# Kernel tuning notes

Measured on AMD Instinct MI355X. Metric: run time of the kernel, lower is better.

The kernel has to match this reference:

```python
import jax, jax.numpy as jnp
import numpy as np

N, E, D_IN, D_HID, D_OUT, R, B = 50000, 600000, 128, 128, 128, 8, 4


def setup_inputs() -> dict:
    key = jax.random.key(0)
    ks = jax.random.split(key, 12)
    s = 0.05
    return {
        "x": jax.random.normal(ks[0], (N, D_IN), jnp.float32),
        "edge_index": jax.random.randint(ks[1], (2, E), 0, N, jnp.int32),
        "edge_type": jax.random.randint(ks[2], (E,), 0, R, jnp.int32),
        "basis1": jax.random.normal(ks[3], (B, D_IN, D_HID), jnp.float32) * s,
        "comp1": jax.random.normal(ks[4], (R, B), jnp.float32) * s,
        "root1": jax.random.normal(ks[5], (D_IN, D_HID), jnp.float32) * s,
        "bias1": jnp.zeros((D_HID,), jnp.float32),
        "basis2": jax.random.normal(ks[6], (B, D_HID, D_OUT), jnp.float32) * s,
        "comp2": jax.random.normal(ks[7], (R, B), jnp.float32) * s,
        "root2": jax.random.normal(ks[8], (D_HID, D_OUT), jnp.float32) * s,
        "bias2": jnp.zeros((D_OUT,), jnp.float32),
    }


def _rgcn_conv(x, src, dst, etype, basis, comp, root, bias):
    # PyG RGCNConv (basis decomposition, aggr='mean' per relation):
    # out_i = x_i @ root + bias + sum_r mean_{e: type=r, dst=i} (x_src_e @ W_r)
    # W_r linear => aggregate raw features per (node, relation), then transform.
    n = x.shape[0]
    r = comp.shape[0]
    W = jnp.einsum('rb,bio->rio', comp, basis)          # [R, in, out]
    seg = dst * r + etype                               # [E] composite key
    agg = jax.ops.segment_sum(x[src], seg, num_segments=n * r)        # [N*R, in]
    cnt = jax.ops.segment_sum(jnp.ones_like(seg, x.dtype), seg, num_segments=n * r)
    mean = (agg / jnp.maximum(cnt, 1.0)[:, None]).reshape(n, r, -1)   # [N, R, in]
    return jnp.einsum('nri,rio->no', mean, W) + x @ root + bias


def reference(x, edge_index, edge_type, basis1, comp1, root1, bias1,
              basis2, comp2, root2, bias2):
    src, dst = edge_index[0], edge_index[1]
    h = _rgcn_conv(x, src, dst, edge_type, basis1, comp1, root1, bias1)
    h = jax.nn.relu(h)
    # dropout p=0.2 is identity in eval mode
    out = _rgcn_conv(h, src, dst, edge_type, basis2, comp2, root2, bias2)
    return out
```

## Files before the change

kernel.cpp:

```cpp
#include <hip/hip_runtime.h>

#define NN 50000
#define NE 600000
#define DD 128
#define RR 8
#define NBASIS 4
#define NR (NN * RR)
#define KTOT 640
#define MPAD 50048

typedef float f32x4 __attribute__((ext_vector_type(4)));
typedef short bf16x8 __attribute__((ext_vector_type(8)));

static __device__ __forceinline__ unsigned short f2b(float f) {
  union { float f; unsigned u; } c; c.f = f;
  unsigned u = c.u + 0x7fffu + ((c.u >> 16) & 1u);
  return (unsigned short)(u >> 16);
}
static __device__ __forceinline__ unsigned pack2(float lo, float hi) {
  return (unsigned)f2b(lo) | ((unsigned)f2b(hi) << 16);
}
static __device__ __forceinline__ float b2f_lo(unsigned v) {
  union { unsigned u; float f; } c; c.u = v << 16; return c.f;
}
static __device__ __forceinline__ float b2f_hi(unsigned v) {
  union { unsigned u; float f; } c; c.u = v & 0xffff0000u; return c.f;
}

__global__ __launch_bounds__(256) void count_kernel(
    const int* __restrict__ dst, const int* __restrict__ et,
    int* __restrict__ cnt) {
  int e = blockIdx.x * 256 + threadIdx.x;
  if (e < NE) atomicAdd(&cnt[dst[e] * RR + et[e]], 1);
}

__global__ __launch_bounds__(256) void scan1_kernel(
    const int* __restrict__ cnt, int* __restrict__ deg,
    int* __restrict__ offs, int* __restrict__ partials) {
  __shared__ int s[256];
  int t = threadIdx.x;
  int i = blockIdx.x * 256 + t;
  int v = 0;
  if (i < NN) {
    const int4* c4 = (const int4*)cnt;
    int4 a = c4[i * 2];
    int4 b = c4[i * 2 + 1];
    v = a.x + a.y + a.z + a.w + b.x + b.y + b.z + b.w;
    deg[i] = v;
  }
  s[t] = v;
  __syncthreads();
  for (int off = 1; off < 256; off <<= 1) {
    int add = (t >= off) ? s[t - off] : 0;
    __syncthreads();
    s[t] += add;
    __syncthreads();
  }
  if (i < NN) offs[i] = s[t] - v;
  if (t == 255) partials[blockIdx.x] = s[255];
}

__global__ __launch_bounds__(256) void scan2_kernel(
    int* __restrict__ partials, int nb) {
  __shared__ int s[256];
  int t = threadIdx.x;
  int v = (t < nb) ? partials[t] : 0;
  s[t] = v;
  __syncthreads();
  for (int off = 1; off < 256; off <<= 1) {
    int add = (t >= off) ? s[t - off] : 0;
    __syncthreads();
    s[t] += add;
    __syncthreads();
  }
  if (t < nb) partials[t] = s[t] - v;
}

__global__ __launch_bounds__(256) void scan3_kernel(
    int* __restrict__ offs, const int* __restrict__ partials,
    int* __restrict__ cursor) {
  int i = blockIdx.x * 256 + threadIdx.x;
  if (i < NN) {
    int o = offs[i] + partials[blockIdx.x];
    offs[i] = o;
    cursor[i] = o;
  }
}

__global__ __launch_bounds__(256) void sort_kernel(
    const int* __restrict__ src, const int* __restrict__ dst,
    const int* __restrict__ et, const int* __restrict__ cnt,
    int* __restrict__ cursor, int* __restrict__ skey,
    float* __restrict__ sinv) {
  int e = blockIdx.x * 256 + threadIdx.x;
  if (e >= NE) return;
  int d = dst[e];
  int t = et[e];
  int p = atomicAdd(&cursor[d], 1);
  skey[p] = src[e] | (t << 28);
  sinv[p] = 1.0f / (float)cnt[d * RR + t];
}

__global__ __launch_bounds__(256) void scv_kernel(
    const int* __restrict__ skey, const float* __restrict__ sinv,
    const float* __restrict__ comp1, const float* __restrict__ comp2,
    float4* __restrict__ scv1, float4* __restrict__ scv2) {
  int e = blockIdx.x * 256 + threadIdx.x;
  if (e >= NE) return;
  int t = ((unsigned)skey[e]) >> 28;
  float iv = sinv[e];
  scv1[e] = make_float4(iv * comp1[t * NBASIS + 0], iv * comp1[t * NBASIS + 1],
                        iv * comp1[t * NBASIS + 2], iv * comp1[t * NBASIS + 3]);
  scv2[e] = make_float4(iv * comp2[t * NBASIS + 0], iv * comp2[t * NBASIS + 1],
                        iv * comp2[t * NBASIS + 2], iv * comp2[t * NBASIS + 3]);
}

__global__ __launch_bounds__(256) void tobf16_kernel(
    const float* __restrict__ in, unsigned* __restrict__ outb, int npairs) {
  int i = blockIdx.x * 256 + threadIdx.x;
  if (i < npairs) {
    float2 v = ((const float2*)in)[i];
    outb[i] = pack2(v.x, v.y);
  }
}

__global__ __launch_bounds__(256) void btbuild_kernel(
    const float* __restrict__ basis, const float* __restrict__ root,
    unsigned short* __restrict__ BT) {
  int idx = blockIdx.x * 256 + threadIdx.x;
  if (idx >= DD * KTOT) return;
  int c = idx / KTOT;
  int k = idx - c * KTOT;
  float v = (k < 512) ? basis[(size_t)((k >> 7) * DD + (k & 127)) * DD + c]
                      : root[(size_t)(k - 512) * DD + c];
  BT[idx] = f2b(v);
}

__global__ __launch_bounds__(256) void agg_kernel(
    const uint4* __restrict__ featb4,
    const int* __restrict__ skey, const float4* __restrict__ scv,
    const int* __restrict__ offs, const int* __restrict__ deg,
    uint4* __restrict__ Ab4) {
  int node = blockIdx.x * 4 + (threadIdx.x >> 6);
  if (node >= NN) return;
  int lane = threadIdx.x & 63;
  int g = lane >> 4;
  int q = lane & 15;

  float a0[8] = {}, a1[8] = {}, a2[8] = {}, a3[8] = {};

  int beg = offs[node];
  int dg = deg[node];
  for (int i = g; i < dg; i += 4) {
    int key = skey[beg + i];
    int s = key & 0x0FFFFFFF;
    float4 c = scv[beg + i];
    uint4 v = featb4[(size_t)s * 16 + q];
    float e[8];
    e[0] = b2f_lo(v.x); e[1] = b2f_hi(v.x);
    e[2] = b2f_lo(v.y); e[3] = b2f_hi(v.y);
    e[4] = b2f_lo(v.z); e[5] = b2f_hi(v.z);
    e[6] = b2f_lo(v.w); e[7] = b2f_hi(v.w);
#pragma unroll
    for (int j = 0; j < 8; ++j) {
      a0[j] += c.x * e[j];
      a1[j] += c.y * e[j];
      a2[j] += c.z * e[j];
      a3[j] += c.w * e[j];
    }
  }

#pragma unroll
  for (int j = 0; j < 8; ++j) {
    a0[j] += __shfl_xor(a0[j], 16); a0[j] += __shfl_xor(a0[j], 32);
    a1[j] += __shfl_xor(a1[j], 16); a1[j] += __shfl_xor(a1[j], 32);
    a2[j] += __shfl_xor(a2[j], 16); a2[j] += __shfl_xor(a2[j], 32);
    a3[j] += __shfl_xor(a3[j], 16); a3[j] += __shfl_xor(a3[j], 32);
  }

  uint4* row = Ab4 + (size_t)node * 80;
  uint4 w;
  if (g == 0) {
    w.x = pack2(a0[0], a0[1]); w.y = pack2(a0[2], a0[3]);
    w.z = pack2(a0[4], a0[5]); w.w = pack2(a0[6], a0[7]);
  } else if (g == 1) {
    w.x = pack2(a1[0], a1[1]); w.y = pack2(a1[2], a1[3]);
    w.z = pack2(a1[4], a1[5]); w.w = pack2(a1[6], a1[7]);
  } else if (g == 2) {
    w.x = pack2(a2[0], a2[1]); w.y = pack2(a2[2], a2[3]);
    w.z = pack2(a2[4], a2[5]); w.w = pack2(a2[6], a2[7]);
  } else {
    w.x = pack2(a3[0], a3[1]); w.y = pack2(a3[2], a3[3]);
    w.z = pack2(a3[4], a3[5]); w.w = pack2(a3[6], a3[7]);
  }
  row[g * 16 + q] = w;
  if (g == 0) row[64 + q] = featb4[(size_t)node * 16 + q];
}

template <int OUT_BF16>
__global__ __launch_bounds__(256) void gemm_mfma(
    const unsigned short* __restrict__ Ab, const unsigned short* __restrict__ BT,
    const float* __restrict__ bias, void* __restrict__ Cout) {
  __shared__ unsigned short As[128][64];
  __shared__ unsigned short Bs[128][64];

  int tid = threadIdx.x;
  int row0 = blockIdx.x * 128;
  int lane = tid & 63;
  int wid = tid >> 6;
  int wr = (wid >> 1) * 64;
  int wc = (wid & 1) * 64;

  f32x4 acc[4][4] = {};

  for (int kt = 0; kt < KTOT; kt += 64) {
#pragma unroll
    for (int i = 0; i < 4; ++i) {
      int off = i * 256 + tid;
      int r = off >> 3;
      int ke = (off & 7) << 3;
      *(uint4*)((unsigned short*)As + (size_t)off * 8) =
          *(const uint4*)(Ab + (size_t)(row0 + r) * KTOT + kt + ke);
      *(uint4*)((unsigned short*)Bs + (size_t)off * 8) =
          *(const uint4*)(BT + (size_t)r * KTOT + kt + ke);
    }
    __syncthreads();

#pragma unroll
    for (int kk = 0; kk < 2; ++kk) {
      int ko = kk * 32 + ((lane >> 4) << 3);
      bf16x8 a[4], b[4];
#pragma unroll
      for (int m = 0; m < 4; ++m)
        a[m] = *(const bf16x8*)&As[wr + m * 16 + (lane & 15)][ko];
#pragma unroll
      for (int n = 0; n < 4; ++n)
        b[n] = *(const bf16x8*)&Bs[wc + n * 16 + (lane & 15)][ko];
#pragma unroll
      for (int m = 0; m < 4; ++m)
#pragma unroll
        for (int n = 0; n < 4; ++n)
          acc[m][n] = __builtin_amdgcn_mfma_f32_16x16x32_bf16(
              a[m], b[n], acc[m][n], 0, 0, 0);
    }
    __syncthreads();
  }

#pragma unroll
  for (int n = 0; n < 4; ++n) {
    int col = wc + n * 16 + (lane & 15);
    float bb = bias[col];
#pragma unroll
    for (int m = 0; m < 4; ++m) {
      f32x4 v = acc[m][n];
#pragma unroll
      for (int j = 0; j < 4; ++j) {
        int row = row0 + wr + m * 16 + ((lane >> 4) << 2) + j;
        if (row < NN) {
          float o = v[j] + bb;
          if (OUT_BF16) {
            o = fmaxf(o, 0.f);
            ((unsigned short*)Cout)[(size_t)row * DD + col] = f2b(o);
          } else {
            ((float*)Cout)[(size_t)row * DD + col] = o;
          }
        }
      }
    }
  }
}

extern "C" void kernel_launch(void* const* d_in, const int* in_sizes, int n_in,
                              void* d_out, int out_size, void* d_ws,
                              size_t ws_size, hipStream_t stream) {
  const float* x      = (const float*)d_in[0];
  const int*   eidx   = (const int*)d_in[1];
  const int*   etype  = (const int*)d_in[2];
  const float* basis1 = (const float*)d_in[3];
  const float* comp1  = (const float*)d_in[4];
  const float* root1  = (const float*)d_in[5];
  const float* bias1  = (const float*)d_in[6];
  const float* basis2 = (const float*)d_in[7];
  const float* comp2  = (const float*)d_in[8];
  const float* root2  = (const float*)d_in[9];
  const float* bias2  = (const float*)d_in[10];
  float* out = (float*)d_out;

  const int* src = eidx;
  const int* dst = eidx + NE;

  unsigned short* Ab  = (unsigned short*)d_ws;
  unsigned short* hb  = Ab + (size_t)MPAD * KTOT;
  unsigned short* xb  = hb + (size_t)NN * DD;
  unsigned short* BT1 = xb + (size_t)NN * DD;
  unsigned short* BT2 = BT1 + (size_t)DD * KTOT;
  float4* scv1 = (float4*)(BT2 + (size_t)DD * KTOT);
  float4* scv2 = scv1 + NE;
  float* sinv = (float*)(scv2 + NE);
  int*   skey = (int*)(sinv + NE);
  int*   cnt  = skey + NE;
  int*   deg  = cnt + NR;
  int*   offs = deg + NN;
  int*   curs = offs + NN;
  int*   part = curs + NN;

  const int NB = (NN + 255) / 256;
  const int EB = (NE + 255) / 256;

  hipMemsetAsync(cnt, 0, (size_t)NR * sizeof(int), stream);
  count_kernel<<<EB, 256, 0, stream>>>(dst, etype, cnt);
  scan1_kernel<<<NB, 256, 0, stream>>>(cnt, deg, offs, part);
  scan2_kernel<<<1, 256, 0, stream>>>(part, NB);
  scan3_kernel<<<NB, 256, 0, stream>>>(offs, part, curs);
  sort_kernel<<<EB, 256, 0, stream>>>(src, dst, etype, cnt, curs, skey, sinv);
  scv_kernel<<<EB, 256, 0, stream>>>(skey, sinv, comp1, comp2, scv1, scv2);

  tobf16_kernel<<<(NN * DD / 2 + 255) / 256, 256, 0, stream>>>(
      x, (unsigned*)xb, NN * DD / 2);
  btbuild_kernel<<<(DD * KTOT + 255) / 256, 256, 0, stream>>>(basis1, root1, BT1);
  btbuild_kernel<<<(DD * KTOT + 255) / 256, 256, 0, stream>>>(basis2, root2, BT2);

  int agg_blocks = (NN + 3) / 4;
  int gemm_blocks = MPAD / 128;

  agg_kernel<<<agg_blocks, 256, 0, stream>>>((const uint4*)xb, skey, scv1,
                                             offs, deg, (uint4*)Ab);
  gemm_mfma<1><<<gemm_blocks, 256, 0, stream>>>(Ab, BT1, bias1, hb);

  agg_kernel<<<agg_blocks, 256, 0, stream>>>((const uint4*)hb, skey, scv2,
                                             offs, deg, (uint4*)Ab);
  gemm_mfma<0><<<gemm_blocks, 256, 0, stream>>>(Ab, BT2, bias2, out);
}
```

Baseline: 258.7 us.

## Fuse aggregation with MFMA GEMM per node tile and merge preprocessing kernels

Replaces the separate aggregation and GEMM kernels with one fused kernel per layer. It aggregates 16 nodes into LDS and immediately runs MFMA against the basis/root matrix read from global memory, which removes the large intermediate A buffer round trip. Preprocessing launches (bf16 conversion, BT build, edge counting) are merged into one kernel. The three-pass scan becomes a single pass that takes block bases from an atomic counter, so node segments are no longer in node order. Per-edge coefficient arrays are dropped in favour of per-node relation coefficients computed in shared memory. The cost is a small 16-row GEMM tile that rereads BT from global memory for every block, and lower MFMA reuse.

```diff
diff --git a/kernel.cpp b/kernel.cpp
--- a/kernel.cpp
+++ b/kernel.cpp
@@ -7,7 +7,7 @@
 #define NBASIS 4
 #define NR (NN * RR)
 #define KTOT 640
-#define MPAD 50048
+#define NPB 16
 
 typedef float f32x4 __attribute__((ext_vector_type(4)));
 typedef short bf16x8 __attribute__((ext_vector_type(8)));
@@ -27,17 +27,47 @@
   union { unsigned u; float f; } c; c.u = v & 0xffff0000u; return c.f;
 }
 
-__global__ __launch_bounds__(256) void count_kernel(
-    const int* __restrict__ dst, const int* __restrict__ et,
+#define PREP_XB 12500
+#define PREP_BT 320
+#define PREP_CNT 2344
+#define PREP_TOTAL (PREP_XB + 2 * PREP_BT + PREP_CNT)
+
+__global__ __launch_bounds__(256) void prep_kernel(
+    const float* __restrict__ x, const float* __restrict__ basis1,
+    const float* __restrict__ root1, const float* __restrict__ basis2,
+    const float* __restrict__ root2, const int* __restrict__ dst,
+    const int* __restrict__ et, unsigned* __restrict__ xb,
+    unsigned short* __restrict__ BT1, unsigned short* __restrict__ BT2,
     int* __restrict__ cnt) {
-  int e = blockIdx.x * 256 + threadIdx.x;
-  if (e < NE) atomicAdd(&cnt[dst[e] * RR + et[e]], 1);
-}
-
-__global__ __launch_bounds__(256) void scan1_kernel(
-    const int* __restrict__ cnt, int* __restrict__ deg,
-    int* __restrict__ offs, int* __restrict__ partials) {
+  int bid = blockIdx.x;
+  int t = threadIdx.x;
+  if (bid < PREP_XB) {
+    int i = bid * 256 + t;
+    float2 v = ((const float2*)x)[i];
+    xb[i] = pack2(v.x, v.y);
+  } else if (bid < PREP_XB + PREP_BT) {
+    int idx = (bid - PREP_XB) * 256 + t;
+    int c = idx / KTOT, k = idx - c * KTOT;
+    float v = (k < 512) ? basis1[(size_t)((k >> 7) * DD + (k & 127)) * DD + c]
+                        : root1[(size_t)(k - 512) * DD + c];
+    BT1[idx] = f2b(v);
+  } else if (bid < PREP_XB + 2 * PREP_BT) {
+    int idx = (bid - PREP_XB - PREP_BT) * 256 + t;
+    int c = idx / KTOT, k = idx - c * KTOT;
+    float v = (k < 512) ? basis2[(size_t)((k >> 7) * DD + (k & 127)) * DD + c]
+                        : root2[(size_t)(k - 512) * DD + c];
+    BT2[idx] = f2b(v);
+  } else {
+    int e = (bid - PREP_XB - 2 * PREP_BT) * 256 + t;
+    if (e < NE) atomicAdd(&cnt[dst[e] * RR + et[e]], 1);
+  }
+}
+
+__global__ __launch_bounds__(256) void offs_kernel(
+    const int* __restrict__ cnt, int2* __restrict__ od,
+    int* __restrict__ curs, int* __restrict__ gcur) {
   __shared__ int s[256];
+  __shared__ int base;
   int t = threadIdx.x;
   int i = blockIdx.x * 256 + t;
   int v = 0;
@@ -46,7 +76,6 @@
     int4 a = c4[i * 2];
     int4 b = c4[i * 2 + 1];
     v = a.x + a.y + a.z + a.w + b.x + b.y + b.z + b.w;
-    deg[i] = v;
   }
   s[t] = v;
   __syncthreads();
@@ -56,216 +85,138 @@
     s[t] += add;
     __syncthreads();
   }
-  if (i < NN) offs[i] = s[t] - v;
-  if (t == 255) partials[blockIdx.x] = s[255];
-}
-
-__global__ __launch_bounds__(256) void scan2_kernel(
-    int* __restrict__ partials, int nb) {
-  __shared__ int s[256];
-  int t = threadIdx.x;
-  int v = (t < nb) ? partials[t] : 0;
-  s[t] = v;
-  __syncthreads();
-  for (int off = 1; off < 256; off <<= 1) {
-    int add = (t >= off) ? s[t - off] : 0;
-    __syncthreads();
-    s[t] += add;
-    __syncthreads();
-  }
-  if (t < nb) partials[t] = s[t] - v;
-}
-
-__global__ __launch_bounds__(256) void scan3_kernel(
-    int* __restrict__ offs, const int* __restrict__ partials,
-    int* __restrict__ cursor) {
-  int i = blockIdx.x * 256 + threadIdx.x;
+  if (t == 255) base = atomicAdd(gcur, s[255]);
+  __syncthreads();
   if (i < NN) {
-    int o = offs[i] + partials[blockIdx.x];
-    offs[i] = o;
-    cursor[i] = o;
+    int o = base + s[t] - v;
+    od[i] = make_int2(o, v);
+    curs[i] = o;
   }
 }
 
 __global__ __launch_bounds__(256) void sort_kernel(
     const int* __restrict__ src, const int* __restrict__ dst,
-    const int* __restrict__ et, const int* __restrict__ cnt,
-    int* __restrict__ cursor, int* __restrict__ skey,
-    float* __restrict__ sinv) {
+    const int* __restrict__ et, int* __restrict__ curs,
+    int* __restrict__ skey) {
   int e = blockIdx.x * 256 + threadIdx.x;
   if (e >= NE) return;
-  int d = dst[e];
-  int t = et[e];
-  int p = atomicAdd(&cursor[d], 1);
-  skey[p] = src[e] | (t << 28);
-  sinv[p] = 1.0f / (float)cnt[d * RR + t];
-}
-
-__global__ __launch_bounds__(256) void scv_kernel(
-    const int* __restrict__ skey, const float* __restrict__ sinv,
-    const float* __restrict__ comp1, const float* __restrict__ comp2,
-    float4* __restrict__ scv1, float4* __restrict__ scv2) {
-  int e = blockIdx.x * 256 + threadIdx.x;
-  if (e >= NE) return;
-  int t = ((unsigned)skey[e]) >> 28;
-  float iv = sinv[e];
-  scv1[e] = make_float4(iv * comp1[t * NBASIS + 0], iv * comp1[t * NBASIS + 1],
-                        iv * comp1[t * NBASIS + 2], iv * comp1[t * NBASIS + 3]);
-  scv2[e] = make_float4(iv * comp2[t * NBASIS + 0], iv * comp2[t * NBASIS + 1],
-                        iv * comp2[t * NBASIS + 2], iv * comp2[t * NBASIS + 3]);
-}
-
-__global__ __launch_bounds__(256) void tobf16_kernel(
-    const float* __restrict__ in, unsigned* __restrict__ outb, int npairs) {
-  int i = blockIdx.x * 256 + threadIdx.x;
-  if (i < npairs) {
-    float2 v = ((const float2*)in)[i];
-    outb[i] = pack2(v.x, v.y);
-  }
-}
-
-__global__ __launch_bounds__(256) void btbuild_kernel(
-    const float* __restrict__ basis, const float* __restrict__ root,
-    unsigned short* __restrict__ BT) {
-  int idx = blockIdx.x * 256 + threadIdx.x;
-  if (idx >= DD * KTOT) return;
-  int c = idx / KTOT;
-  int k = idx - c * KTOT;
-  float v = (k < 512) ? basis[(size_t)((k >> 7) * DD + (k & 127)) * DD + c]
-                      : root[(size_t)(k - 512) * DD + c];
-  BT[idx] = f2b(v);
-}
-
-__global__ __launch_bounds__(256) void agg_kernel(
+  int p = atomicAdd(&curs[dst[e]], 1);
+  skey[p] = src[e] | (et[e] << 28);
+}
+
+template <int OUT_BF16>
+__global__ __launch_bounds__(512, 6) void rgcn_fused(
     const uint4* __restrict__ featb4,
-    const int* __restrict__ skey, const float4* __restrict__ scv,
-    const int* __restrict__ offs, const int* __restrict__ deg,
-    uint4* __restrict__ Ab4) {
-  int node = blockIdx.x * 4 + (threadIdx.x >> 6);
-  if (node >= NN) return;
-  int lane = threadIdx.x & 63;
+    const int* __restrict__ skey, const int* __restrict__ cnt,
+    const float* __restrict__ comp, const int2* __restrict__ od,
+    const unsigned short* __restrict__ BT,
+    const float* __restrict__ bias, void* __restrict__ Cout) {
+  __shared__ unsigned short zl[NPB][648];
+  __shared__ float compl_[RR * NBASIS];
+  __shared__ float ccl[NPB][RR * NBASIS];
+
+  int tid = threadIdx.x;
+  if (tid < RR * NBASIS) compl_[tid] = comp[tid];
+  __syncthreads();
+
+  int wid = tid >> 6;
+  int lane = tid & 63;
   int g = lane >> 4;
   int q = lane & 15;
-
-  float a0[8] = {}, a1[8] = {}, a2[8] = {}, a3[8] = {};
-
-  int beg = offs[node];
-  int dg = deg[node];
-  for (int i = g; i < dg; i += 4) {
-    int key = skey[beg + i];
-    int s = key & 0x0FFFFFFF;
-    float4 c = scv[beg + i];
-    uint4 v = featb4[(size_t)s * 16 + q];
-    float e[8];
-    e[0] = b2f_lo(v.x); e[1] = b2f_hi(v.x);
-    e[2] = b2f_lo(v.y); e[3] = b2f_hi(v.y);
-    e[4] = b2f_lo(v.z); e[5] = b2f_hi(v.z);
-    e[6] = b2f_lo(v.w); e[7] = b2f_hi(v.w);
+  int nb = blockIdx.x * NPB;
+
+  for (int r0 = 0; r0 < 2; ++r0) {
+    int row = wid * 2 + r0;
+    int node = nb + row;
+    int2 o_d = od[node];
+    int beg = o_d.x, dg = o_d.y;
+
+    if (lane < 32) {
+      int c = cnt[node * RR + (lane >> 2)];
+      ccl[row][lane] = compl_[lane] * (1.0f / (float)max(c, 1));
+    }
+
+    float a0[8] = {}, a1[8] = {}, a2[8] = {}, a3[8] = {};
+    for (int i = g; i < dg; i += 8) {
+      int k1 = skey[beg + i];
+      bool has2 = (i + 4 < dg);
+      int k2 = has2 ? skey[beg + i + 4] : k1;
+      int t1 = ((unsigned)k1) >> 28;
+      int t2 = ((unsigned)k2) >> 28;
+      uint4 v1 = featb4[(size_t)(k1 & 0x0FFFFFFF) * 16 + q];
+      uint4 v2 = featb4[(size_t)(k2 & 0x0FFFFFFF) * 16 + q];
+      float c10 = ccl[row][t1 * 4 + 0], c11 = ccl[row][t1 * 4 + 1];
+      float c12 = ccl[row][t1 * 4 + 2], c13 = ccl[row][t1 * 4 + 3];
+      float sc2 = has2 ? 1.0f : 0.0f;
+      float c20 = sc2 * ccl[row][t2 * 4 + 0], c21 = sc2 * ccl[row][t2 * 4 + 1];
+      float c22 = sc2 * ccl[row][t2 * 4 + 2], c23 = sc2 * ccl[row][t2 * 4 + 3];
+      float e1[8], e2[8];
+      e1[0] = b2f_lo(v1.x); e1[1] = b2f_hi(v1.x);
+      e1[2] = b2f_lo(v1.y); e1[3] = b2f_hi(v1.y);
+      e1[4] = b2f_lo(v1.z); e1[5] = b2f_hi(v1.z);
+      e1[6] = b2f_lo(v1.w); e1[7] = b2f_hi(v1.w);
+      e2[0] = b2f_lo(v2.x); e2[1] = b2f_hi(v2.x);
+      e2[2] = b2f_lo(v2.y); e2[3] = b2f_hi(v2.y);
+      e2[4] = b2f_lo(v2.z); e2[5] = b2f_hi(v2.z);
+      e2[6] = b2f_lo(v2.w); e2[7] = b2f_hi(v2.w);
+#pragma unroll
+      for (int j = 0; j < 8; ++j) {
+        a0[j] += c10 * e1[j] + c20 * e2[j];
+        a1[j] += c11 * e1[j] + c21 * e2[j];
+        a2[j] += c12 * e1[j] + c22 * e2[j];
+        a3[j] += c13 * e1[j] + c23 * e2[j];
+      }
+    }
+
 #pragma unroll
     for (int j = 0; j < 8; ++j) {
-      a0[j] += c.x * e[j];
-      a1[j] += c.y * e[j];
-      a2[j] += c.z * e[j];
-      a3[j] += c.w * e[j];
-    }
-  }
-
+      a0[j] += __shfl_xor(a0[j], 16); a0[j] += __shfl_xor(a0[j], 32);
+      a1[j] += __shfl_xor(a1[j], 16); a1[j] += __shfl_xor(a1[j], 32);
+      a2[j] += __shfl_xor(a2[j], 16); a2[j] += __shfl_xor(a2[j], 32);
+      a3[j] += __shfl_xor(a3[j], 16); a3[j] += __shfl_xor(a3[j], 32);
+    }
+
+    uint4 w;
+    if (g == 0) {
+      w.x = pack2(a0[0], a0[1]); w.y = pack2(a0[2], a0[3]);
+      w.z = pack2(a0[4], a0[5]); w.w = pack2(a0[6], a0[7]);
+    } else if (g == 1) {
+      w.x = pack2(a1[0], a1[1]); w.y = pack2(a1[2], a1[3]);
+      w.z = pack2(a1[4], a1[5]); w.w = pack2(a1[6], a1[7]);
+    } else if (g == 2) {
+      w.x = pack2(a2[0], a2[1]); w.y = pack2(a2[2], a2[3]);
+      w.z = pack2(a2[4], a2[5]); w.w = pack2(a2[6], a2[7]);
+    } else {
+      w.x = pack2(a3[0], a3[1]); w.y = pack2(a3[2], a3[3]);
+      w.z = pack2(a3[4], a3[5]); w.w = pack2(a3[6], a3[7]);
+    }
+    *(uint4*)&zl[row][g * 128 + q * 8] = w;
+    if (g == 0)
+      *(uint4*)&zl[row][512 + q * 8] = featb4[(size_t)node * 16 + q];
+  }
+  __syncthreads();
+
+  f32x4 acc = {};
+#pragma unroll 4
+  for (int ks = 0; ks < 20; ++ks) {
+    int ko = ks * 32 + ((lane >> 4) << 3);
+    bf16x8 af = *(const bf16x8*)&zl[lane & 15][ko];
+    bf16x8 bf_ =
+        *(const bf16x8*)(BT + (size_t)(wid * 16 + (lane & 15)) * KTOT + ko);
+    acc = __builtin_amdgcn_mfma_f32_16x16x32_bf16(af, bf_, acc, 0, 0, 0);
+  }
+
+  int col = wid * 16 + (lane & 15);
+  float bb = bias[col];
 #pragma unroll
-  for (int j = 0; j < 8; ++j) {
-    a0[j] += __shfl_xor(a0[j], 16); a0[j] += __shfl_xor(a0[j], 32);
-    a1[j] += __shfl_xor(a1[j], 16); a1[j] += __shfl_xor(a1[j], 32);
-    a2[j] += __shfl_xor(a2[j], 16); a2[j] += __shfl_xor(a2[j], 32);
-    a3[j] += __shfl_xor(a3[j], 16); a3[j] += __shfl_xor(a3[j], 32);
-  }
-
-  uint4* row = Ab4 + (size_t)node * 80;
-  uint4 w;
-  if (g == 0) {
-    w.x = pack2(a0[0], a0[1]); w.y = pack2(a0[2], a0[3]);
-    w.z = pack2(a0[4], a0[5]); w.w = pack2(a0[6], a0[7]);
-  } else if (g == 1) {
-    w.x = pack2(a1[0], a1[1]); w.y = pack2(a1[2], a1[3]);
-    w.z = pack2(a1[4], a1[5]); w.w = pack2(a1[6], a1[7]);
-  } else if (g == 2) {
-    w.x = pack2(a2[0], a2[1]); w.y = pack2(a2[2], a2[3]);
-    w.z = pack2(a2[4], a2[5]); w.w = pack2(a2[6], a2[7]);
-  } else {
-    w.x = pack2(a3[0], a3[1]); w.y = pack2(a3[2], a3[3]);
-    w.z = pack2(a3[4], a3[5]); w.w = pack2(a3[6], a3[7]);
-  }
-  row[g * 16 + q] = w;
-  if (g == 0) row[64 + q] = featb4[(size_t)node * 16 + q];
-}
-
-template <int OUT_BF16>
-__global__ __launch_bounds__(256) void gemm_mfma(
-    const unsigned short* __restrict__ Ab, const unsigned short* __restrict__ BT,
-    const float* __restrict__ bias, void* __restrict__ Cout) {
-  __shared__ unsigned short As[128][64];
-  __shared__ unsigned short Bs[128][64];
-
-  int tid = threadIdx.x;
-  int row0 = blockIdx.x * 128;
-  int lane = tid & 63;
-  int wid = tid >> 6;
-  int wr = (wid >> 1) * 64;
-  int wc = (wid & 1) * 64;
-
-  f32x4 acc[4][4] = {};
-
-  for (int kt = 0; kt < KTOT; kt += 64) {
-#pragma unroll
-    for (int i = 0; i < 4; ++i) {
-      int off = i * 256 + tid;
-      int r = off >> 3;
-      int ke = (off & 7) << 3;
-      *(uint4*)((unsigned short*)As + (size_t)off * 8) =
-          *(const uint4*)(Ab + (size_t)(row0 + r) * KTOT + kt + ke);
-      *(uint4*)((unsigned short*)Bs + (size_t)off * 8) =
-          *(const uint4*)(BT + (size_t)r * KTOT + kt + ke);
-    }
-    __syncthreads();
-
-#pragma unroll
-    for (int kk = 0; kk < 2; ++kk) {
-      int ko = kk * 32 + ((lane >> 4) << 3);
-      bf16x8 a[4], b[4];
-#pragma unroll
-      for (int m = 0; m < 4; ++m)
-        a[m] = *(const bf16x8*)&As[wr + m * 16 + (lane & 15)][ko];
-#pragma unroll
-      for (int n = 0; n < 4; ++n)
-        b[n] = *(const bf16x8*)&Bs[wc + n * 16 + (lane & 15)][ko];
-#pragma unroll
-      for (int m = 0; m < 4; ++m)
-#pragma unroll
-        for (int n = 0; n < 4; ++n)
-          acc[m][n] = __builtin_amdgcn_mfma_f32_16x16x32_bf16(
-              a[m], b[n], acc[m][n], 0, 0, 0);
-    }
-    __syncthreads();
-  }
-
-#pragma unroll
-  for (int n = 0; n < 4; ++n) {
-    int col = wc + n * 16 + (lane & 15);
-    float bb = bias[col];
-#pragma unroll
-    for (int m = 0; m < 4; ++m) {
-      f32x4 v = acc[m][n];
-#pragma unroll
-      for (int j = 0; j < 4; ++j) {
-        int row = row0 + wr + m * 16 + ((lane >> 4) << 2) + j;
-        if (row < NN) {
-          float o = v[j] + bb;
-          if (OUT_BF16) {
-            o = fmaxf(o, 0.f);
-            ((unsigned short*)Cout)[(size_t)row * DD + col] = f2b(o);
-          } else {
-            ((float*)Cout)[(size_t)row * DD + col] = o;
-          }
-        }
-      }
+  for (int j = 0; j < 4; ++j) {
+    int grow = nb + ((lane >> 4) << 2) + j;
+    float o = acc[j] + bb;
+    if (OUT_BF16) {
+      o = fmaxf(o, 0.f);
+      ((unsigned short*)Cout)[(size_t)grow * DD + col] = f2b(o);
+    } else {
+      ((float*)Cout)[(size_t)grow * DD + col] = o;
     }
   }
 }
@@ -289,45 +240,28 @@
   const int* src = eidx;
   const int* dst = eidx + NE;
 
-  unsigned short* Ab  = (unsigned short*)d_ws;
-  unsigned short* hb  = Ab + (size_t)MPAD * KTOT;
-  unsigned short* xb  = hb + (size_t)NN * DD;
-  unsigned short* BT1 = xb + (size_t)NN * DD;
+  unsigned short* xb  = (unsigned short*)d_ws;
+  unsigned short* hb  = xb + (size_t)NN * DD;
+  unsigned short* BT1 = hb + (size_t)NN * DD;
   unsigned short* BT2 = BT1 + (size_t)DD * KTOT;
-  float4* scv1 = (float4*)(BT2 + (size_t)DD * KTOT);
-  float4* scv2 = scv1 + NE;
-  float* sinv = (float*)(scv2 + NE);
-  int*   skey = (int*)(sinv + NE);
-  int*   cnt  = skey + NE;
-  int*   deg  = cnt + NR;
-  int*   offs = deg + NN;
-  int*   curs = offs + NN;
-  int*   part = curs + NN;
+  int*  skey = (int*)(BT2 + (size_t)DD * KTOT);
+  int*  cnt  = skey + NE;
+  int*  gcur = cnt + NR;
+  int2* od   = (int2*)(gcur + 4);
+  int*  curs = (int*)(od + NN);
 
   const int NB = (NN + 255) / 256;
   const int EB = (NE + 255) / 256;
 
-  hipMemsetAsync(cnt, 0, (size_t)NR * sizeof(int), stream);
-  count_kernel<<<EB, 256, 0, stream>>>(dst, etype, cnt);
-  scan1_kernel<<<NB, 256, 0, stream>>>(cnt, deg, offs, part);
-  scan2_kernel<<<1, 256, 0, stream>>>(part, NB);
-  scan3_kernel<<<NB, 256, 0, stream>>>(offs, part, curs);
-  sort_kernel<<<EB, 256, 0, stream>>>(src, dst, etype, cnt, curs, skey, sinv);
-  scv_kernel<<<EB, 256, 0, stream>>>(skey, sinv, comp1, comp2, scv1, scv2);
-
-  tobf16_kernel<<<(NN * DD / 2 + 255) / 256, 256, 0, stream>>>(
-      x, (unsigned*)xb, NN * DD / 2);
-  btbuild_kernel<<<(DD * KTOT + 255) / 256, 256, 0, stream>>>(basis1, root1, BT1);
-  btbuild_kernel<<<(DD * KTOT + 255) / 256, 256, 0, stream>>>(basis2, root2, BT2);
-
-  int agg_blocks = (NN + 3) / 4;
-  int gemm_blocks = MPAD / 128;
-
-  agg_kernel<<<agg_blocks, 256, 0, stream>>>((const uint4*)xb, skey, scv1,
-                                             offs, deg, (uint4*)Ab);
-  gemm_mfma<1><<<gemm_blocks, 256, 0, stream>>>(Ab, BT1, bias1, hb);
-
-  agg_kernel<<<agg_blocks, 256, 0, stream>>>((const uint4*)hb, skey, scv2,
-                                             offs, deg, (uint4*)Ab);
-  gemm_mfma<0><<<gemm_blocks, 256, 0, stream>>>(Ab, BT2, bias2, out);
-}
+  hipMemsetAsync(cnt, 0, (size_t)(NR + 4) * sizeof(int), stream);
+  prep_kernel<<<PREP_TOTAL, 256, 0, stream>>>(
+      x, basis1, root1, basis2, root2, dst, etype, (unsigned*)xb, BT1, BT2,
+      cnt);
+  offs_kernel<<<NB, 256, 0, stream>>>(cnt, od, curs, gcur);
+  sort_kernel<<<EB, 256, 0, stream>>>(src, dst, etype, curs, skey);
+
+  rgcn_fused<1><<<NN / NPB, 512, 0, stream>>>((const uint4*)xb, skey, cnt,
+                                              comp1, od, BT1, bias1, hb);
+  rgcn_fused<0><<<NN / NPB, 512, 0, stream>>>((const uint4*)hb, skey, cnt,
+                                              comp2, od, BT2, bias2, out);
+}
```

Measured after the change: 318.4 us. 1.23x slower.
